# Kernel tuning notes

Hardware: AMD Instinct MI355X
Metric: run time of the kernel (lower is better)

## Reference

```python
import jax, jax.numpy as jnp
import numpy as np
from jax import lax

D = 30   # embedding_dim (hardcoded in repo)
Q = 30   # question length
N = 4000 # number of sentences in doc
S = 100  # tokens per sentence
K = 5    # k_for_maxpool
SLOPE = 0.1  # LeakyReLU negative slope


def setup_inputs() -> dict:
    key = jax.random.key(0)
    ks = jax.random.split(key, 20)
    rn = lambda k, sh: jax.random.normal(k, sh, dtype=jnp.float32)
    ru = lambda k, sh: jax.random.uniform(k, sh, dtype=jnp.float32)
    return {
        "doc_sents_embeds": rn(ks[0], (N, S, D)),
        "sents_gaf": ru(ks[1], (N, 3)),
        "question_embeds": rn(ks[2], (Q, D)),
        "q_idfs": ru(ks[3], (Q, 1)),
        "doc_gaf": ru(ks[4], (4,)),
        "conv1_w": rn(ks[5], (D, D, 3)) * 0.1,
        "conv1_b": rn(ks[6], (D,)) * 0.1,
        "conv2_w": rn(ks[7], (D, D, 3)) * 0.1,
        "conv2_b": rn(ks[8], (D,)) * 0.1,
        "qw_W": rn(ks[9], (1, D + 1)) * 0.1,
        "qw_b": rn(ks[10], (1,)) * 0.1,
        "lq1_W": rn(ks[11], (8, 6)) * 0.1,
        "lq1_b": rn(ks[12], (8,)) * 0.1,
        "lq2_W": rn(ks[13], (1, 8)) * 0.1,
        "lq2_b": rn(ks[14], (1,)) * 0.1,
        "so_W": rn(ks[15], (1, 4)) * 0.1,
        "so_b": rn(ks[16], (1,)) * 0.1,
        "fl_W": rn(ks[17], (1, 5)) * 0.1,
        "fl_b": rn(ks[18], (1,)) * 0.1,
    }


def _leaky(x):
    return jnp.where(x >= 0, x, SLOPE * x)


def _conv_block(x, w, b):
    # x: [B, L, D]. torch Conv1d(D, D, 3, padding=2) then slice [1:L+1]
    # is exactly a 'same' conv with padding 1 on each side; then residual add.
    y = lax.conv_general_dilated(x.transpose(0, 2, 1), w, (1,), [(1, 1)],
                                 dimension_numbers=("NCH", "OIH", "NCH"))
    y = _leaky(y + b[None, :, None])
    return y.transpose(0, 2, 1) + x


def _cos_sim(A, B):
    # A: [Q, D], B: [N, S, D] -> [N, Q, S] (num/den as in torch my_cosine_sim)
    num = jnp.einsum("qd,nsd->nqs", A, B)
    den = jnp.linalg.norm(A, axis=-1)[None, :, None] * jnp.linalg.norm(B, axis=-1)[:, None, :]
    return num / den


def _pool(sim):
    # sort-based k-max pooling -> [max, avg_of_top_k]; sim: [N, Q, S] -> [N, Q, 2]
    vals = lax.top_k(sim, K)[0]  # descending
    return jnp.stack([vals[..., 0], vals.mean(-1)], axis=-1)


def reference(doc_sents_embeds, sents_gaf, question_embeds, q_idfs, doc_gaf,
              conv1_w, conv1_b, conv2_w, conv2_b, qw_W, qw_b,
              lq1_W, lq1_b, lq2_W, lq2_b, so_W, so_b, fl_W, fl_b):
    # question context (two residual trigram convs)
    q_conv = _conv_block(question_embeds[None], conv1_w, conv1_b)
    q_conv = _conv_block(q_conv, conv2_w, conv2_b)[0]          # [Q, D]
    # question term weights
    qw_in = jnp.concatenate([q_conv, q_idfs], axis=-1)          # [Q, D+1]
    q_weights = jax.nn.softmax((qw_in @ qw_W.T + qw_b)[:, 0])   # [Q]
    # sentence context convs (batched over all sentences)
    conv_res = _conv_block(doc_sents_embeds, conv1_w, conv1_b)
    conv_res = _conv_block(conv_res, conv2_w, conv2_b)          # [N, S, D]
    # similarity matrices
    sim_insens = _cos_sim(question_embeds, doc_sents_embeds)    # [N, Q, S]
    sim_oh = (sim_insens > 1.0 - 1e-3).astype(sim_insens.dtype)
    sim_sens = _cos_sim(q_conv, conv_res)
    # k-max pooling and per-q tiny MLP attention
    feats = jnp.concatenate([_pool(sim_oh), _pool(sim_insens), _pool(sim_sens)], axis=-1)  # [N, Q, 6]
    lo = _leaky(feats @ lq1_W.T + lq1_b) @ lq2_W.T + lq2_b      # [N, Q, 1]
    lo = lo[..., 0] * q_weights[None, :]
    sent_emit = lo.sum(-1) / Q                                  # [N]
    # per-sentence output layer
    sent_feats = jnp.concatenate([sents_gaf, sent_emit[:, None]], axis=-1)  # [N, 4]
    sent_scores = jax.nn.sigmoid((sent_feats @ so_W.T + so_b)[:, 0])        # [N]
    # doc-level score
    doc_rep = jnp.concatenate([jnp.max(sent_scores)[None], doc_gaf])        # [5]
    final = doc_rep @ fl_W.T + fl_b                                          # [1]
    return final, sent_scores
```

## Files before the change

kernel.cpp:

```cpp
#include <hip/hip_runtime.h>
#include <hip/hip_bf16.h>

#define SLOPE 0.1f

#define OFF_QW    1816
#define OFF_QNI   1846
#define OFF_QNS   1876
#define OFF_B1    4606
#define OFF_B2    7336
#define OFF_LQ1W  7366
#define OFF_LQ1B  7414
#define OFF_LQ2W  7422
#define OFF_LQ2B  7430
#define OFF_SOW   7431
#define OFF_SOB   7435
#define OFF_FLW   7436
#define OFF_FLB   7441
#define U16_QEA   16384
#define U16_QCA   17408
#define U16_WB1   18432
#define U16_WB2   21504

typedef __attribute__((ext_vector_type(8))) __bf16 bf16x8;
typedef __attribute__((ext_vector_type(4))) float f32x4;

union Frag { uint4 u4; uint u[4]; bf16x8 v; };

__device__ __forceinline__ float bf2f(ushort h) {
    union { uint u; float f; } c; c.u = ((uint)h) << 16; return c.f;
}
__device__ __forceinline__ ushort f2bf(float f) {
    union { float f; uint u; } c; c.f = f;
    uint u = c.u;
    return (ushort)((u + 0x7FFFu + ((u >> 16) & 1u)) >> 16);
}
__device__ __forceinline__ float ldx(const void* p, long i, int bf) {
    if (bf) return bf2f(((const ushort*)p)[i]);
    return ((const float*)p)[i];
}

__global__ __launch_bounds__(256) void k_detect(const unsigned short* p, int* flag) {
    __shared__ int cnt;
    int tid = threadIdx.x;
    if (tid == 0) cnt = 0;
    __syncthreads();
    int local = 0;
    for (int i = tid; i < 4096; i += 256) {
        unsigned e = (p[i] >> 7) & 0xFFu;
        if (e != 0u && (e < 100u || e > 134u)) local++;
    }
    atomicAdd(&cnt, local);
    __syncthreads();
    if (tid == 0) flag[0] = (cnt > 200) ? 0 : 1;
}

__global__ __launch_bounds__(256) void k_question(
        const void* qe_in, const void* qidf_in,
        const void* w1_in, const void* b1_in,
        const void* w2_in, const void* b2_in,
        const void* qwW_in, const void* qwb_in,
        const void* lq1W_in, const void* lq1b_in,
        const void* lq2W_in, const void* lq2b_in,
        const void* soW_in, const void* sob_in,
        const void* flW_in, const void* flb_in,
        float* ws) {
    const int tid = threadIdx.x;
    const int bf = ((const int*)ws)[0];
    __shared__ float QE[900], T1[900], QC[900], W[2700], IDF[32], LG[32];

    if (tid < 30) { ws[OFF_B1 + tid] = ldx(b1_in, tid, bf);
                    ws[OFF_B2 + tid] = ldx(b2_in, tid, bf); }
    if (tid < 48) ws[OFF_LQ1W + tid] = ldx(lq1W_in, tid, bf);
    if (tid < 8)  { ws[OFF_LQ1B + tid] = ldx(lq1b_in, tid, bf);
                    ws[OFF_LQ2W + tid] = ldx(lq2W_in, tid, bf); }
    if (tid < 4)  ws[OFF_SOW + tid] = ldx(soW_in, tid, bf);
    if (tid < 5)  ws[OFF_FLW + tid] = ldx(flW_in, tid, bf);
    if (tid == 0) { ws[OFF_LQ2B] = ldx(lq2b_in, 0, bf);
                    ws[OFF_SOB]  = ldx(sob_in, 0, bf);
                    ws[OFF_FLB]  = ldx(flb_in, 0, bf); }

    for (int i = tid; i < 900; i += 256) QE[i] = ldx(qe_in, i, bf);
    if (tid < 30) IDF[tid] = ldx(qidf_in, tid, bf);
    for (int i = tid; i < 2700; i += 256) W[i] = ldx(w1_in, i, bf);
    __syncthreads();

    for (int idx = tid; idx < 900; idx += 256) {
        int s = idx / 30, o = idx % 30;
        float acc = ldx(b1_in, o, bf);
        for (int k = 0; k < 3; ++k) {
            int t = s + k - 1;
            if (t < 0 || t >= 30) continue;
            for (int i = 0; i < 30; ++i) acc += QE[t*30 + i] * W[o*90 + i*3 + k];
        }
        acc = acc >= 0.f ? acc : SLOPE * acc;
        T1[idx] = acc + QE[idx];
    }
    __syncthreads();
    for (int i = tid; i < 2700; i += 256) W[i] = ldx(w2_in, i, bf);
    __syncthreads();
    for (int idx = tid; idx < 900; idx += 256) {
        int s = idx / 30, o = idx % 30;
        float acc = ldx(b2_in, o, bf);
        for (int k = 0; k < 3; ++k) {
            int t = s + k - 1;
            if (t < 0 || t >= 30) continue;
            for (int i = 0; i < 30; ++i) acc += T1[t*30 + i] * W[o*90 + i*3 + k];
        }
        acc = acc >= 0.f ? acc : SLOPE * acc;
        QC[idx] = acc + T1[idx];
    }
    __syncthreads();

    if (tid < 30) {
        float s1 = 0.f, s2 = 0.f;
        for (int d = 0; d < 30; ++d) {
            float a = QE[tid*30 + d]; s1 += a*a;
            float b = QC[tid*30 + d]; s2 += b*b;
        }
        ws[OFF_QNI + tid] = 1.0f / sqrtf(s1);
        ws[OFF_QNS + tid] = 1.0f / sqrtf(s2);
        float z = ldx(qwb_in, 0, bf);
        for (int d = 0; d < 30; ++d) z += QC[tid*30 + d] * ldx(qwW_in, d, bf);
        z += IDF[tid] * ldx(qwW_in, 30, bf);
        LG[tid] = z;
    }
    __syncthreads();
    if (tid == 0) {
        float m = -1e30f;
        for (int q = 0; q < 30; ++q) m = fmaxf(m, LG[q]);
        float sum = 0.f, e[30];
        for (int q = 0; q < 30; ++q) { e[q] = expf(LG[q] - m); sum += e[q]; }
        for (int q = 0; q < 30; ++q) ws[OFF_QW + q] = e[q] / sum;
    }

    ushort* wsu = (ushort*)ws;
    for (int i = tid; i < 1024; i += 256) {
        int q = i >> 5, d = i & 31;
        float ve = (q < 30 && d < 30) ? QE[q*30 + d] : 0.f;
        float vc = (q < 30 && d < 30) ? QC[q*30 + d] : 0.f;
        wsu[U16_QEA + i] = f2bf(ve);
        wsu[U16_QCA + i] = f2bf(vc);
    }
    for (int i = tid; i < 3072; i += 256) {
        int o = i / 96, kk = i % 96;
        float v1 = 0.f, v2 = 0.f;
        if (o < 30 && kk < 90) {
            int ii = kk % 30, k = kk / 30;
            v1 = ldx(w1_in, o*90 + ii*3 + k, bf);
            v2 = ldx(w2_in, o*90 + ii*3 + k, bf);
        }
        wsu[U16_WB1 + i] = f2bf(v1);
        wsu[U16_WB2 + i] = f2bf(v2);
    }
}

__device__ __forceinline__ void conv_tile(const uint* src32, const uint4* wb,
                                          const float* bias, int t, int l15, int quad) {
    const ushort* srcU = (const ushort*)src32;
    int mt = t >> 1, nt = t & 1;
    int sa = mt * 16 + l15;
    f32x4 acc = {0.f, 0.f, 0.f, 0.f};
    Frag a, b;
    for (int k = 0; k < 3; ++k) {
        if (sa < 100) {
            int base = sa * 15 + k * 16 + quad * 4;
            a.u[0] = src32[base];     a.u[1] = src32[base + 1];
            a.u[2] = src32[base + 2]; a.u[3] = src32[base + 3];
        } else { a.u[0] = a.u[1] = a.u[2] = a.u[3] = 0u; }
        b.u4 = wb[(nt * 16 + l15) * 12 + k * 4 + quad];
        acc = __builtin_amdgcn_mfma_f32_16x16x32_bf16(a.v, b.v, acc, 0, 0, 0);
    }
    int o = nt * 16 + l15;
    (void)o; (void)srcU; (void)bias; (void)acc;
}

__device__ __forceinline__ void conv_tile_rw(const uint* src32, uint* dst32, const uint4* wb,
                                             const float* bias, int t, int l15, int quad) {
    const ushort* srcU = (const ushort*)src32;
    ushort* dstU = (ushort*)dst32;
    int mt = t >> 1, nt = t & 1;
    int sa = mt * 16 + l15;
    f32x4 acc = {0.f, 0.f, 0.f, 0.f};
    Frag a, b;
    for (int k = 0; k < 3; ++k) {
        if (sa < 100) {
            int base = sa * 15 + k * 16 + quad * 4;
            a.u[0] = src32[base];     a.u[1] = src32[base + 1];
            a.u[2] = src32[base + 2]; a.u[3] = src32[base + 3];
        } else { a.u[0] = a.u[1] = a.u[2] = a.u[3] = 0u; }
        b.u4 = wb[(nt * 16 + l15) * 12 + k * 4 + quad];
        acc = __builtin_amdgcn_mfma_f32_16x16x32_bf16(a.v, b.v, acc, 0, 0, 0);
    }
    int o = nt * 16 + l15;
    if (o < 30) {
        float bo = bias[o];
        for (int r = 0; r < 4; ++r) {
            int s = mt * 16 + quad * 4 + r;
            if (s < 100) {
                float v = acc[r] + bo;
                v = v >= 0.f ? v : SLOPE * v;
                v += bf2f(srcU[(s + 1) * 30 + o]);
                dstU[(s + 1) * 30 + o] = f2bf(v);
            }
        }
    }
}

__device__ __forceinline__ void sim_tile(const uint4* qa, const uint* src32, float* SIMb,
                                         const float* invq, const float* INVX,
                                         int t, int l15, int quad) {
    int mt = t / 7, nt = t % 7;
    Frag a, b;
    a.u4 = qa[(mt * 16 + l15) * 4 + quad];
    int s = nt * 16 + l15;
    if (s < 100) {
        int base = (s + 1) * 15 + quad * 4;
        b.u[0] = src32[base];     b.u[1] = src32[base + 1];
        b.u[2] = src32[base + 2]; b.u[3] = src32[base + 3];
    } else { b.u[0] = b.u[1] = b.u[2] = b.u[3] = 0u; }
    f32x4 acc = {0.f, 0.f, 0.f, 0.f};
    acc = __builtin_amdgcn_mfma_f32_16x16x32_bf16(a.v, b.v, acc, 0, 0, 0);
    if (s < 100) {
        float ix = INVX[s];
        for (int r = 0; r < 4; ++r) {
            int q = mt * 16 + quad * 4 + r;
            if (q < 30) SIMb[q * 101 + s] = acc[r] * invq[q] * ix;
        }
    }
}

__device__ __forceinline__ void pool_wave(const float* SIMb, float* fe,
                                          int lane, int fbase, int do_oh) {
    int qr = lane & 31;
    int q = qr < 30 ? qr : 0;
    int half = lane >> 5;
    const float* row = SIMb + q * 101 + half * 50;
    float t0=-1e30f, t1=-1e30f, t2=-1e30f, t3=-1e30f, t4=-1e30f;
    int cnt = 0;
    for (int s = 0; s < 50; ++s) {
        float v = row[s];
        cnt += (v > 0.999f) ? 1 : 0;
        bool b0 = v > t0, b1 = v > t1, b2 = v > t2, b3 = v > t3, b4 = v > t4;
        float n0 = b0 ? v  : t0;
        float n1 = b0 ? t0 : (b1 ? v : t1);
        float n2 = b1 ? t1 : (b2 ? v : t2);
        float n3 = b2 ? t2 : (b3 ? v : t3);
        float n4 = b3 ? t3 : (b4 ? v : t4);
        t0=n0; t1=n1; t2=n2; t3=n3; t4=n4;
    }
    float pv[5];
    pv[0] = __shfl_xor(t0, 32); pv[1] = __shfl_xor(t1, 32); pv[2] = __shfl_xor(t2, 32);
    pv[3] = __shfl_xor(t3, 32); pv[4] = __shfl_xor(t4, 32);
    int pc = __shfl_xor(cnt, 32);
    for (int j = 0; j < 5; ++j) {
        float v = pv[j];
        bool b0 = v > t0, b1 = v > t1, b2 = v > t2, b3 = v > t3, b4 = v > t4;
        float n0 = b0 ? v  : t0;
        float n1 = b0 ? t0 : (b1 ? v : t1);
        float n2 = b1 ? t1 : (b2 ? v : t2);
        float n3 = b2 ? t2 : (b3 ? v : t3);
        float n4 = b3 ? t3 : (b4 ? v : t4);
        t0=n0; t1=n1; t2=n2; t3=n3; t4=n4;
    }
    cnt += pc;
    if (do_oh) {
        fe[0] = cnt > 0 ? 1.f : 0.f;
        fe[1] = (float)(cnt > 5 ? 5 : cnt) * 0.2f;
    }
    fe[fbase]     = t0;
    fe[fbase + 1] = (t0 + t1 + t2 + t3 + t4) * 0.2f;
}

__global__ __launch_bounds__(256) void k_main(const void* doc_in, const void* gaf_in,
                                              void* out, float* ws) {
    const int n = blockIdx.x;
    const int tid = threadIdx.x;
    const int bf = ((const int*)ws)[0];
    const int lane = tid & 63;
    const int wid = tid >> 6;
    const int l15 = lane & 15;
    const int quad = lane >> 4;

    __shared__ uint XA32[1546];
    __shared__ uint XB32[1546];
    __shared__ float SIM[3030];
    __shared__ float INVX[100];
    __shared__ float RED[32];

    ushort* XAu = (ushort*)XA32;
    const ushort* wsu = (const ushort*)ws;
    const uint4* qeA = (const uint4*)(wsu + U16_QEA);
    const uint4* qcA = (const uint4*)(wsu + U16_QCA);
    const uint4* wb1 = (const uint4*)(wsu + U16_WB1);
    const uint4* wb2 = (const uint4*)(wsu + U16_WB2);

    for (int i = tid; i < 15; i += 256) { XA32[i] = 0u; XB32[i] = 0u; }
    for (int i = 1515 + tid; i < 1546; i += 256) { XA32[i] = 0u; XB32[i] = 0u; }
    if (bf) {
        const uint* g = (const uint*)((const ushort*)doc_in + (size_t)n * 3000);
        for (int i = tid; i < 1500; i += 256) XA32[15 + i] = g[i];
    } else {
        const float* p = (const float*)doc_in + (size_t)n * 3000;
        for (int i = tid; i < 3000; i += 256) XAu[30 + i] = f2bf(p[i]);
    }
    __syncthreads();

    if (tid < 100) {
        const uint* r = XA32 + (tid + 1) * 15;
        float s = 0.f;
        for (int i = 0; i < 15; ++i) {
            uint u = r[i];
            float lo = __uint_as_float(u << 16);
            float hi = __uint_as_float(u & 0xFFFF0000u);
            s += lo * lo + hi * hi;
        }
        INVX[tid] = 1.f / sqrtf(s);
    }
    __syncthreads();

    for (int t = wid; t < 14; t += 4)
        sim_tile(qeA, XA32, SIM, ws + OFF_QNI, INVX, t, l15, quad);
    __syncthreads();

    float fe[6];
    if (wid == 0) {
        pool_wave(SIM, fe, lane, 2, 1);
    } else {
        for (int t = wid - 1; t < 14; t += 3)
            conv_tile_rw(XA32, XB32, wb1, ws + OFF_B1, t, l15, quad);
    }
    __syncthreads();

    for (int t = wid; t < 14; t += 4)
        conv_tile_rw(XB32, XA32, wb2, ws + OFF_B2, t, l15, quad);
    __syncthreads();

    if (tid < 100) {
        const uint* r = XA32 + (tid + 1) * 15;
        float s = 0.f;
        for (int i = 0; i < 15; ++i) {
            uint u = r[i];
            float lo = __uint_as_float(u << 16);
            float hi = __uint_as_float(u & 0xFFFF0000u);
            s += lo * lo + hi * hi;
        }
        INVX[tid] = 1.f / sqrtf(s);
    }
    __syncthreads();

    for (int t = wid; t < 14; t += 4)
        sim_tile(qcA, XA32, SIM, ws + OFF_QNS, INVX, t, l15, quad);
    __syncthreads();

    if (wid == 0) {
        pool_wave(SIM, fe, lane, 4, 0);
        if (lane < 30) {
            float lo = ws[OFF_LQ2B];
            for (int j = 0; j < 8; ++j) {
                float h = ws[OFF_LQ1B + j];
                for (int f = 0; f < 6; ++f) h += fe[f] * ws[OFF_LQ1W + j*6 + f];
                h = h >= 0.f ? h : SLOPE * h;
                lo += h * ws[OFF_LQ2W + j];
            }
            RED[lane] = lo * ws[OFF_QW + lane];
        }
    }
    __syncthreads();

    if (tid == 0) {
        float emit = 0.f;
        for (int q = 0; q < 30; ++q) emit += RED[q];
        emit *= (1.f / 30.f);
        float z = ws[OFF_SOB];
        z += ldx(gaf_in, (long)n*3 + 0, bf) * ws[OFF_SOW + 0];
        z += ldx(gaf_in, (long)n*3 + 1, bf) * ws[OFF_SOW + 1];
        z += ldx(gaf_in, (long)n*3 + 2, bf) * ws[OFF_SOW + 2];
        z += emit * ws[OFF_SOW + 3];
        float sc = 1.f / (1.f + expf(-z));
        if (bf) ((__hip_bfloat16*)out)[1 + n] = __float2bfloat16(sc);
        else    ((float*)out)[1 + n] = sc;
    }
}

__global__ __launch_bounds__(256) void k_final(const void* docgaf_in, void* out, const float* ws) {
    const int tid = threadIdx.x;
    const int bf = ((const int*)ws)[0];
    __shared__ float red[256];
    float m = -1e30f;
    for (int i = tid; i < 4000; i += 256) {
        float v = bf ? __bfloat162float(((const __hip_bfloat16*)out)[1 + i])
                     : ((const float*)out)[1 + i];
        m = fmaxf(m, v);
    }
    red[tid] = m;
    __syncthreads();
    for (int off = 128; off > 0; off >>= 1) {
        if (tid < off) red[tid] = fmaxf(red[tid], red[tid + off]);
        __syncthreads();
    }
    if (tid == 0) {
        float f = ws[OFF_FLB] + red[0] * ws[OFF_FLW + 0];
        for (int i = 0; i < 4; ++i) f += ldx(docgaf_in, i, bf) * ws[OFF_FLW + 1 + i];
        if (bf) ((__hip_bfloat16*)out)[0] = __float2bfloat16(f);
        else    ((float*)out)[0] = f;
    }
}

extern "C" void kernel_launch(void* const* d_in, const int* in_sizes, int n_in,
                              void* d_out, int out_size, void* d_ws, size_t ws_size,
                              hipStream_t stream) {
    float* ws = (float*)d_ws;
    k_detect<<<1, 256, 0, stream>>>((const unsigned short*)d_in[0], (int*)d_ws);
    k_question<<<1, 256, 0, stream>>>(d_in[2], d_in[3], d_in[5], d_in[6], d_in[7], d_in[8],
                                      d_in[9], d_in[10], d_in[11], d_in[12], d_in[13], d_in[14],
                                      d_in[15], d_in[16], d_in[17], d_in[18], ws);
    k_main<<<4000, 256, 0, stream>>>(d_in[0], d_in[1], d_out, ws);
    k_final<<<1, 256, 0, stream>>>(d_in[4], d_out, ws);
}
```

Measured before the change: 212.4 us.

## Fuse detect/question/final kernels and parallelize k-max pooling across all waves

Merges the dtype-detect kernel into the question-prep kernel and folds the final doc-level max reduction into the main kernel using an atomic counter so the last block computes it, cutting the launch count from four to two. Pooling is moved from a single wave to all 256 threads: each 8-thread group scans one query row and the partial top-5 lists are merged with shuffles. The first conv then runs on all four waves rather than three, and the per-query sum becomes a wave shuffle reduction. This adds a threadfence and an atomic per block, plus one more block-wide barrier.

```diff
diff --git a/kernel.cpp b/kernel.cpp
--- a/kernel.cpp
+++ b/kernel.cpp
@@ -38,23 +38,19 @@
     if (bf) return bf2f(((const ushort*)p)[i]);
     return ((const float*)p)[i];
 }
-
-__global__ __launch_bounds__(256) void k_detect(const unsigned short* p, int* flag) {
-    __shared__ int cnt;
-    int tid = threadIdx.x;
-    if (tid == 0) cnt = 0;
-    __syncthreads();
-    int local = 0;
-    for (int i = tid; i < 4096; i += 256) {
-        unsigned e = (p[i] >> 7) & 0xFFu;
-        if (e != 0u && (e < 100u || e > 134u)) local++;
-    }
-    atomicAdd(&cnt, local);
-    __syncthreads();
-    if (tid == 0) flag[0] = (cnt > 200) ? 0 : 1;
-}
-
-__global__ __launch_bounds__(256) void k_question(
+__device__ __forceinline__ void top5_insert(float v, float& t0, float& t1,
+                                            float& t2, float& t3, float& t4) {
+    bool b0 = v > t0, b1 = v > t1, b2 = v > t2, b3 = v > t3, b4 = v > t4;
+    float n0 = b0 ? v  : t0;
+    float n1 = b0 ? t0 : (b1 ? v : t1);
+    float n2 = b1 ? t1 : (b2 ? v : t2);
+    float n3 = b2 ? t2 : (b3 ? v : t3);
+    float n4 = b3 ? t3 : (b4 ? v : t4);
+    t0 = n0; t1 = n1; t2 = n2; t3 = n3; t4 = n4;
+}
+
+__global__ __launch_bounds__(256) void k_prep(
+        const void* doc_in,
         const void* qe_in, const void* qidf_in,
         const void* w1_in, const void* b1_in,
         const void* w2_in, const void* b2_in,
@@ -65,8 +61,23 @@
         const void* flW_in, const void* flb_in,
         float* ws) {
     const int tid = threadIdx.x;
-    const int bf = ((const int*)ws)[0];
     __shared__ float QE[900], T1[900], QC[900], W[2700], IDF[32], LG[32];
+    __shared__ int scnt;
+
+    if (tid == 0) scnt = 0;
+    __syncthreads();
+    {
+        const ushort* p = (const ushort*)doc_in;
+        int local = 0;
+        for (int i = tid; i < 4096; i += 256) {
+            unsigned e = (p[i] >> 7) & 0xFFu;
+            if (e != 0u && (e < 100u || e > 134u)) local++;
+        }
+        atomicAdd(&scnt, local);
+    }
+    __syncthreads();
+    const int bf = (scnt > 200) ? 0 : 1;
+    if (tid == 0) { ((int*)ws)[0] = bf; ((int*)ws)[1] = 0; }
 
     if (tid < 30) { ws[OFF_B1 + tid] = ldx(b1_in, tid, bf);
                     ws[OFF_B2 + tid] = ldx(b2_in, tid, bf); }
@@ -152,26 +163,6 @@
         wsu[U16_WB1 + i] = f2bf(v1);
         wsu[U16_WB2 + i] = f2bf(v2);
     }
-}
-
-__device__ __forceinline__ void conv_tile(const uint* src32, const uint4* wb,
-                                          const float* bias, int t, int l15, int quad) {
-    const ushort* srcU = (const ushort*)src32;
-    int mt = t >> 1, nt = t & 1;
-    int sa = mt * 16 + l15;
-    f32x4 acc = {0.f, 0.f, 0.f, 0.f};
-    Frag a, b;
-    for (int k = 0; k < 3; ++k) {
-        if (sa < 100) {
-            int base = sa * 15 + k * 16 + quad * 4;
-            a.u[0] = src32[base];     a.u[1] = src32[base + 1];
-            a.u[2] = src32[base + 2]; a.u[3] = src32[base + 3];
-        } else { a.u[0] = a.u[1] = a.u[2] = a.u[3] = 0u; }
-        b.u4 = wb[(nt * 16 + l15) * 12 + k * 4 + quad];
-        acc = __builtin_amdgcn_mfma_f32_16x16x32_bf16(a.v, b.v, acc, 0, 0, 0);
-    }
-    int o = nt * 16 + l15;
-    (void)o; (void)srcU; (void)bias; (void)acc;
 }
 
 __device__ __forceinline__ void conv_tile_rw(const uint* src32, uint* dst32, const uint4* wb,
@@ -229,50 +220,8 @@
     }
 }
 
-__device__ __forceinline__ void pool_wave(const float* SIMb, float* fe,
-                                          int lane, int fbase, int do_oh) {
-    int qr = lane & 31;
-    int q = qr < 30 ? qr : 0;
-    int half = lane >> 5;
-    const float* row = SIMb + q * 101 + half * 50;
-    float t0=-1e30f, t1=-1e30f, t2=-1e30f, t3=-1e30f, t4=-1e30f;
-    int cnt = 0;
-    for (int s = 0; s < 50; ++s) {
-        float v = row[s];
-        cnt += (v > 0.999f) ? 1 : 0;
-        bool b0 = v > t0, b1 = v > t1, b2 = v > t2, b3 = v > t3, b4 = v > t4;
-        float n0 = b0 ? v  : t0;
-        float n1 = b0 ? t0 : (b1 ? v : t1);
-        float n2 = b1 ? t1 : (b2 ? v : t2);
-        float n3 = b2 ? t2 : (b3 ? v : t3);
-        float n4 = b3 ? t3 : (b4 ? v : t4);
-        t0=n0; t1=n1; t2=n2; t3=n3; t4=n4;
-    }
-    float pv[5];
-    pv[0] = __shfl_xor(t0, 32); pv[1] = __shfl_xor(t1, 32); pv[2] = __shfl_xor(t2, 32);
-    pv[3] = __shfl_xor(t3, 32); pv[4] = __shfl_xor(t4, 32);
-    int pc = __shfl_xor(cnt, 32);
-    for (int j = 0; j < 5; ++j) {
-        float v = pv[j];
-        bool b0 = v > t0, b1 = v > t1, b2 = v > t2, b3 = v > t3, b4 = v > t4;
-        float n0 = b0 ? v  : t0;
-        float n1 = b0 ? t0 : (b1 ? v : t1);
-        float n2 = b1 ? t1 : (b2 ? v : t2);
-        float n3 = b2 ? t2 : (b3 ? v : t3);
-        float n4 = b3 ? t3 : (b4 ? v : t4);
-        t0=n0; t1=n1; t2=n2; t3=n3; t4=n4;
-    }
-    cnt += pc;
-    if (do_oh) {
-        fe[0] = cnt > 0 ? 1.f : 0.f;
-        fe[1] = (float)(cnt > 5 ? 5 : cnt) * 0.2f;
-    }
-    fe[fbase]     = t0;
-    fe[fbase + 1] = (t0 + t1 + t2 + t3 + t4) * 0.2f;
-}
-
 __global__ __launch_bounds__(256) void k_main(const void* doc_in, const void* gaf_in,
-                                              void* out, float* ws) {
+                                              const void* docgaf_in, void* out, float* ws) {
     const int n = blockIdx.x;
     const int tid = threadIdx.x;
     const int bf = ((const int*)ws)[0];
@@ -285,7 +234,8 @@
     __shared__ uint XB32[1546];
     __shared__ float SIM[3030];
     __shared__ float INVX[100];
-    __shared__ float RED[32];
+    __shared__ float FE[30][6];
+    __shared__ int lastflag;
 
     ushort* XAu = (ushort*)XA32;
     const ushort* wsu = (const ushort*)ws;
@@ -293,6 +243,9 @@
     const uint4* qcA = (const uint4*)(wsu + U16_QCA);
     const uint4* wb1 = (const uint4*)(wsu + U16_WB1);
     const uint4* wb2 = (const uint4*)(wsu + U16_WB2);
+
+    const int prow = tid >> 3;
+    const int psub = tid & 7;
 
     for (int i = tid; i < 15; i += 256) { XA32[i] = 0u; XB32[i] = 0u; }
     for (int i = 1515 + tid; i < 1546; i += 256) { XA32[i] = 0u; XB32[i] = 0u; }
@@ -322,13 +275,39 @@
         sim_tile(qeA, XA32, SIM, ws + OFF_QNI, INVX, t, l15, quad);
     __syncthreads();
 
-    float fe[6];
-    if (wid == 0) {
-        pool_wave(SIM, fe, lane, 2, 1);
-    } else {
-        for (int t = wid - 1; t < 14; t += 3)
-            conv_tile_rw(XA32, XB32, wb1, ws + OFF_B1, t, l15, quad);
-    }
+    {
+        float t0=-1e30f, t1=-1e30f, t2=-1e30f, t3=-1e30f, t4=-1e30f;
+        int cnt = 0;
+        if (prow < 30) {
+            const float* r = SIM + prow * 101 + psub * 13;
+            int ne = (psub == 7) ? 9 : 13;
+            for (int i = 0; i < ne; ++i) {
+                float v = r[i];
+                cnt += (v > 0.999f) ? 1 : 0;
+                top5_insert(v, t0, t1, t2, t3, t4);
+            }
+        }
+        for (int d = 1; d < 8; d <<= 1) {
+            float p0 = __shfl_xor(t0, d), p1 = __shfl_xor(t1, d), p2 = __shfl_xor(t2, d);
+            float p3 = __shfl_xor(t3, d), p4 = __shfl_xor(t4, d);
+            cnt += __shfl_xor(cnt, d);
+            top5_insert(p0, t0, t1, t2, t3, t4);
+            top5_insert(p1, t0, t1, t2, t3, t4);
+            top5_insert(p2, t0, t1, t2, t3, t4);
+            top5_insert(p3, t0, t1, t2, t3, t4);
+            top5_insert(p4, t0, t1, t2, t3, t4);
+        }
+        if (prow < 30 && psub == 0) {
+            FE[prow][0] = cnt > 0 ? 1.f : 0.f;
+            FE[prow][1] = (float)(cnt > 5 ? 5 : cnt) * 0.2f;
+            FE[prow][2] = t0;
+            FE[prow][3] = (t0 + t1 + t2 + t3 + t4) * 0.2f;
+        }
+    }
+    __syncthreads();
+
+    for (int t = wid; t < 14; t += 4)
+        conv_tile_rw(XA32, XB32, wb1, ws + OFF_B1, t, l15, quad);
     __syncthreads();
 
     for (int t = wid; t < 14; t += 4)
@@ -352,57 +331,82 @@
         sim_tile(qcA, XA32, SIM, ws + OFF_QNS, INVX, t, l15, quad);
     __syncthreads();
 
+    {
+        float t0=-1e30f, t1=-1e30f, t2=-1e30f, t3=-1e30f, t4=-1e30f;
+        if (prow < 30) {
+            const float* r = SIM + prow * 101 + psub * 13;
+            int ne = (psub == 7) ? 9 : 13;
+            for (int i = 0; i < ne; ++i) top5_insert(r[i], t0, t1, t2, t3, t4);
+        }
+        for (int d = 1; d < 8; d <<= 1) {
+            float p0 = __shfl_xor(t0, d), p1 = __shfl_xor(t1, d), p2 = __shfl_xor(t2, d);
+            float p3 = __shfl_xor(t3, d), p4 = __shfl_xor(t4, d);
+            top5_insert(p0, t0, t1, t2, t3, t4);
+            top5_insert(p1, t0, t1, t2, t3, t4);
+            top5_insert(p2, t0, t1, t2, t3, t4);
+            top5_insert(p3, t0, t1, t2, t3, t4);
+            top5_insert(p4, t0, t1, t2, t3, t4);
+        }
+        if (prow < 30 && psub == 0) {
+            FE[prow][4] = t0;
+            FE[prow][5] = (t0 + t1 + t2 + t3 + t4) * 0.2f;
+        }
+    }
+    __syncthreads();
+
     if (wid == 0) {
-        pool_wave(SIM, fe, lane, 4, 0);
+        float val = 0.f;
         if (lane < 30) {
             float lo = ws[OFF_LQ2B];
             for (int j = 0; j < 8; ++j) {
                 float h = ws[OFF_LQ1B + j];
-                for (int f = 0; f < 6; ++f) h += fe[f] * ws[OFF_LQ1W + j*6 + f];
+                for (int f = 0; f < 6; ++f) h += FE[lane][f] * ws[OFF_LQ1W + j*6 + f];
                 h = h >= 0.f ? h : SLOPE * h;
                 lo += h * ws[OFF_LQ2W + j];
             }
-            RED[lane] = lo * ws[OFF_QW + lane];
-        }
-    }
-    __syncthreads();
-
+            val = lo * ws[OFF_QW + lane];
+        }
+        for (int d = 32; d >= 1; d >>= 1) val += __shfl_xor(val, d);
+        if (lane == 0) {
+            float emit = val * (1.f / 30.f);
+            float z = ws[OFF_SOB];
+            z += ldx(gaf_in, (long)n*3 + 0, bf) * ws[OFF_SOW + 0];
+            z += ldx(gaf_in, (long)n*3 + 1, bf) * ws[OFF_SOW + 1];
+            z += ldx(gaf_in, (long)n*3 + 2, bf) * ws[OFF_SOW + 2];
+            z += emit * ws[OFF_SOW + 3];
+            float sc = 1.f / (1.f + expf(-z));
+            if (bf) ((__hip_bfloat16*)out)[1 + n] = __float2bfloat16(sc);
+            else    ((float*)out)[1 + n] = sc;
+        }
+    }
+
+    __threadfence();
     if (tid == 0) {
-        float emit = 0.f;
-        for (int q = 0; q < 30; ++q) emit += RED[q];
-        emit *= (1.f / 30.f);
-        float z = ws[OFF_SOB];
-        z += ldx(gaf_in, (long)n*3 + 0, bf) * ws[OFF_SOW + 0];
-        z += ldx(gaf_in, (long)n*3 + 1, bf) * ws[OFF_SOW + 1];
-        z += ldx(gaf_in, (long)n*3 + 2, bf) * ws[OFF_SOW + 2];
-        z += emit * ws[OFF_SOW + 3];
-        float sc = 1.f / (1.f + expf(-z));
-        if (bf) ((__hip_bfloat16*)out)[1 + n] = __float2bfloat16(sc);
-        else    ((float*)out)[1 + n] = sc;
-    }
-}
-
-__global__ __launch_bounds__(256) void k_final(const void* docgaf_in, void* out, const float* ws) {
-    const int tid = threadIdx.x;
-    const int bf = ((const int*)ws)[0];
-    __shared__ float red[256];
-    float m = -1e30f;
-    for (int i = tid; i < 4000; i += 256) {
-        float v = bf ? __bfloat162float(((const __hip_bfloat16*)out)[1 + i])
-                     : ((const float*)out)[1 + i];
-        m = fmaxf(m, v);
-    }
-    red[tid] = m;
-    __syncthreads();
-    for (int off = 128; off > 0; off >>= 1) {
-        if (tid < off) red[tid] = fmaxf(red[tid], red[tid + off]);
+        int t = atomicAdd((int*)ws + 1, 1);
+        lastflag = (t == 3999) ? 1 : 0;
+    }
+    __syncthreads();
+    if (lastflag) {
+        __threadfence();
+        float* RED = SIM;
+        float m = -1e30f;
+        for (int i = tid; i < 4000; i += 256) {
+            float v = bf ? __bfloat162float(((const __hip_bfloat16*)out)[1 + i])
+                         : ((const float*)out)[1 + i];
+            m = fmaxf(m, v);
+        }
+        RED[tid] = m;
         __syncthreads();
-    }
-    if (tid == 0) {
-        float f = ws[OFF_FLB] + red[0] * ws[OFF_FLW + 0];
-        for (int i = 0; i < 4; ++i) f += ldx(docgaf_in, i, bf) * ws[OFF_FLW + 1 + i];
-        if (bf) ((__hip_bfloat16*)out)[0] = __float2bfloat16(f);
-        else    ((float*)out)[0] = f;
+        for (int off = 128; off > 0; off >>= 1) {
+            if (tid < off) RED[tid] = fmaxf(RED[tid], RED[tid + off]);
+            __syncthreads();
+        }
+        if (tid == 0) {
+            float f = ws[OFF_FLB] + RED[0] * ws[OFF_FLW + 0];
+            for (int i = 0; i < 4; ++i) f += ldx(docgaf_in, i, bf) * ws[OFF_FLW + 1 + i];
+            if (bf) ((__hip_bfloat16*)out)[0] = __float2bfloat16(f);
+            else    ((float*)out)[0] = f;
+        }
     }
 }
 
@@ -410,10 +414,8 @@
                               void* d_out, int out_size, void* d_ws, size_t ws_size,
                               hipStream_t stream) {
     float* ws = (float*)d_ws;
-    k_detect<<<1, 256, 0, stream>>>((const unsigned short*)d_in[0], (int*)d_ws);
-    k_question<<<1, 256, 0, stream>>>(d_in[2], d_in[3], d_in[5], d_in[6], d_in[7], d_in[8],
-                                      d_in[9], d_in[10], d_in[11], d_in[12], d_in[13], d_in[14],
-                                      d_in[15], d_in[16], d_in[17], d_in[18], ws);
-    k_main<<<4000, 256, 0, stream>>>(d_in[0], d_in[1], d_out, ws);
-    k_final<<<1, 256, 0, stream>>>(d_in[4], d_out, ws);
-}
+    k_prep<<<1, 256, 0, stream>>>(d_in[0], d_in[2], d_in[3], d_in[5], d_in[6], d_in[7], d_in[8],
+                                  d_in[9], d_in[10], d_in[11], d_in[12], d_in[13], d_in[14],
+                                  d_in[15], d_in[16], d_in[17], d_in[18], ws);
+    k_main<<<4000, 256, 0, stream>>>(d_in[0], d_in[1], d_in[4], d_out, ws);
+}
```

Result: slower. 450.1 us (+111.9%).
